# Optimization experiments

Measured on AMD Instinct MI355X. Metric: run time of the kernel, lower is better.

## Reference

```python
import jax, jax.numpy as jnp
import numpy as np

NEG = 0.01  # LeakyReLU negative_slope
N_NODES = 100000
N_EDGES = 400000
D = 128
IN_CH = 16
EDGE_DIM = 1


def _linear(x, w, b):
    # torch.nn.Linear convention: y = x @ W^T + b, W: [out, in]
    return x @ w.T + b


def setup_inputs() -> dict:
    key = jax.random.key(0)
    ks = jax.random.split(key, 32)

    def W(k, o, i):
        return jax.random.normal(k, (o, i), dtype=jnp.float32) * 0.02

    def B(k, o):
        return jax.random.normal(k, (o,), dtype=jnp.float32) * 0.02

    return {
        "x": jax.random.normal(ks[0], (N_NODES, IN_CH), dtype=jnp.float32),
        "edge_index": jax.random.randint(ks[1], (2, N_EDGES), 0, N_NODES, dtype=jnp.int64),
        "edge_weight": jax.random.uniform(ks[2], (N_EDGES, EDGE_DIM), dtype=jnp.float32),
        # prep MLP: in_ch -> 128 (LeakyReLU) -> 128 (Tanh)
        "prep_w0": W(ks[3], D, IN_CH), "prep_b0": B(ks[4], D),
        "prep_w1": W(ks[5], D, D), "prep_b1": B(ks[6], D),
        # GINEConv edge lin: edge_dim -> 128
        "edge_w": W(ks[7], D, EDGE_DIM), "edge_b": B(ks[8], D),
        # GINEConv nn: 128 -> 128 (LReLU) -> 128 (LReLU) -> 128 (Tanh)
        "mlp_w0": W(ks[9], D, D), "mlp_b0": B(ks[10], D),
        "mlp_w1": W(ks[11], D, D), "mlp_b1": B(ks[12], D),
        "mlp_w2": W(ks[13], D, D), "mlp_b2": B(ks[14], D),
        # post MLP: (128+128) -> 128 (LReLU) -> 64 (Tanh)
        "post_w0": W(ks[15], D, 2 * D), "post_b0": B(ks[16], D),
        "post_w1": W(ks[17], 64, D), "post_b1": B(ks[18], 64),
    }


def reference(x, edge_index, edge_weight,
              prep_w0, prep_b0, prep_w1, prep_b1,
              edge_w, edge_b,
              mlp_w0, mlp_b0, mlp_w1, mlp_b1, mlp_w2, mlp_b2,
              post_w0, post_b0, post_w1, post_b1):
    lrelu = lambda v: jax.nn.leaky_relu(v, negative_slope=NEG)
    n = x.shape[0]

    # sequential_prep
    h = lrelu(_linear(x, prep_w0, prep_b0))
    h = jnp.tanh(_linear(h, prep_w1, prep_b1))  # [N, D]

    r = h  # skip connection (x.clone())

    # GINEConv: message = relu(x_j + lin(edge_attr)); aggr = sum per dst
    e = _linear(edge_weight, edge_w, edge_b)            # [E, D]
    m = jax.nn.relu(h[edge_index[0]] + e)               # gather + edge add
    agg = jax.ops.segment_sum(m, edge_index[1], num_segments=n)  # scatter-sum
    z = h + agg  # (1 + eps) * x_i + aggr, eps = 0
    z = lrelu(_linear(z, mlp_w0, mlp_b0))
    z = lrelu(_linear(z, mlp_w1, mlp_b1))
    z = jnp.tanh(_linear(z, mlp_w2, mlp_b2))            # [N, D]

    # skip-cat
    h2 = jnp.concatenate([z, r], axis=1)                # [N, 2D]

    # sequential_post
    o = lrelu(_linear(h2, post_w0, post_b0))
    o = jnp.tanh(_linear(o, post_w1, post_b1))          # [N, 64]
    return o
```

## Files before the change

### kernel.cpp

```cpp
#include <hip/hip_runtime.h>

typedef short bf16x8 __attribute__((ext_vector_type(8)));
typedef float f32x4 __attribute__((ext_vector_type(4)));

#define NEG 0.01f

#define OFF_P0  0
#define OFF_P1  8192
#define OFF_M0  40960
#define OFF_Q0A 139264
#define OFF_Q0B 172032
#define OFF_Q1  204800
#define WBF_BYTES 221184

#define VMCNT0 asm volatile("s_waitcnt vmcnt(0)" ::: "memory")

__device__ __forceinline__ unsigned short f2bf(float f) {
  union { float f; unsigned u; } v; v.f = f;
  unsigned u = v.u;
  return (unsigned short)((u + 0x7fffu + ((u >> 16) & 1u)) >> 16);
}
__device__ __forceinline__ unsigned pack2(float a, float b) {
  return ((unsigned)f2bf(b) << 16) | (unsigned)f2bf(a);
}
__device__ __forceinline__ float bflo(unsigned u) { return __uint_as_float(u << 16); }
__device__ __forceinline__ float bfhi(unsigned u) { return __uint_as_float(u & 0xffff0000u); }
__device__ __forceinline__ float lrelu(float v) { return fmaxf(v, 0.0f) + NEG * fminf(v, 0.0f); }
__device__ __forceinline__ float tanh_fast(float x) {
  float e = __expf(2.0f * x);
  return 1.0f - __fdividef(2.0f, e + 1.0f);
}

__device__ __forceinline__ void gll16(const void* g, void* l) {
  __builtin_amdgcn_global_load_lds((const __attribute__((address_space(1))) void*)g,
                                   (__attribute__((address_space(3))) void*)l, 16, 0, 0);
}

__device__ __forceinline__ void gll_lin(const char* g, char* l, int nchunks, int wv, int nw, int lane) {
  for (int j = wv; j < nchunks; j += nw)
    gll16(g + j * 1024 + lane * 16, l + j * 1024 + lane * 16);
}

__device__ __forceinline__ void gll_rows(const char* gsrc, char* scr, int strip, int N, int lane) {
  #pragma unroll
  for (int c = 0; c < 8; ++c) {
    int L = c * 1024 + lane * 16;
    int row = strip + (L >> 8);
    row = row < N ? row : N - 1;
    gll16(gsrc + (size_t)row * 256 + (L & 255), scr + c * 1024 + lane * 16);
  }
}

__device__ __forceinline__ void copy_rows_out(const char* scr, char* gdst, int strip, int N, int lane) {
  #pragma unroll
  for (int c = 0; c < 8; ++c) {
    int L = c * 1024 + lane * 16;
    int row = strip + (L >> 8);
    if (row < N) *(uint4*)(gdst + (size_t)strip * 256 + L) = *(const uint4*)(scr + L);
  }
}

__device__ __forceinline__ void zacc82(f32x4 acc[8][2]) {
  #pragma unroll
  for (int m = 0; m < 8; ++m)
    #pragma unroll
    for (int n = 0; n < 2; ++n) { f32x4 z = {0.f,0.f,0.f,0.f}; acc[m][n] = z; }
}

__device__ __forceinline__ void gemm128(const char* wbase, const bf16x8 b[2][4],
                                        f32x4 acc[8][2], int l15, int lg) {
  __builtin_amdgcn_s_setprio(1);
  #pragma unroll
  for (int ks = 0; ks < 4; ++ks)
    #pragma unroll
    for (int mf = 0; mf < 8; ++mf) {
      const int row = 16*mf + l15;
      bf16x8 a = *(const bf16x8*)(wbase + row*256 + ((16*lg + 64*ks) ^ ((row&7)<<4)));
      acc[mf][0] = __builtin_amdgcn_mfma_f32_16x16x32_bf16(a, b[0][ks], acc[mf][0], 0,0,0);
      acc[mf][1] = __builtin_amdgcn_mfma_f32_16x16x32_bf16(a, b[1][ks], acc[mf][1], 0,0,0);
    }
  __builtin_amdgcn_s_setprio(0);
}

__device__ __forceinline__ void read_bfrags(const char* scr, bf16x8 b[2][4], int l15, int lg) {
  #pragma unroll
  for (int nf = 0; nf < 2; ++nf) {
    const int n = 16*nf + l15;
    #pragma unroll
    for (int ks = 0; ks < 4; ++ks)
      b[nf][ks] = *(const bf16x8*)(scr + n*256 + ((16*lg + 64*ks) ^ ((n&7)<<4)));
  }
}

template<int ACT>
__device__ __forceinline__ void ep_lds(const f32x4 acc[8][2], const float* __restrict__ bias,
                                       char* scr, int l15, int lg) {
  #pragma unroll
  for (int mf = 0; mf < 8; ++mf) {
    const int ch4 = 16*mf + 4*lg;
    const float4 bv = *(const float4*)(bias + ch4);
    #pragma unroll
    for (int nf = 0; nf < 2; ++nf) {
      const int n = 16*nf + l15;
      float v0 = acc[mf][nf][0]+bv.x, v1 = acc[mf][nf][1]+bv.y;
      float v2 = acc[mf][nf][2]+bv.z, v3 = acc[mf][nf][3]+bv.w;
      if (ACT == 0) { v0=lrelu(v0); v1=lrelu(v1); v2=lrelu(v2); v3=lrelu(v3); }
      else { v0=tanh_fast(v0); v1=tanh_fast(v1); v2=tanh_fast(v2); v3=tanh_fast(v3); }
      uint2 o = { pack2(v0,v1), pack2(v2,v3) };
      *(uint2*)(scr + n*256 + ((32*mf + 8*lg) ^ ((n&7)<<4))) = o;
    }
  }
}

extern "C" __global__ void __launch_bounds__(256) wpack_kernel(
    const float* __restrict__ pw0, const float* __restrict__ pw1,
    const float* __restrict__ mw0, const float* __restrict__ mw1, const float* __restrict__ mw2,
    const float* __restrict__ qw0, const float* __restrict__ qw1,
    char* wbf, int* deg, int N) {
  int gid = blockIdx.x * 256 + threadIdx.x;
  if (gid < 13824) {
    int c = gid;
    const float* src = nullptr;
    int dstB = 0;
    bool zero = false;
    if (c < 512) { int r = c >> 2, q = c & 3;
      dstB = OFF_P0 + r*64 + ((q*16) ^ ((r&3)<<4));
      if (q < 2) src = pw0 + r*16 + q*8; else zero = true;
    } else if (c < 2560) { int i = c - 512, r = i >> 4, q = i & 15;
      dstB = OFF_P1 + r*256 + ((q*16) ^ ((r&7)<<4));
      src = pw1 + r*128 + q*8;
    } else if (c < 8704) { int i = c - 2560, sl = i >> 11, j = i & 2047, r = j >> 4, q = j & 15;
      const float* m = (sl==0) ? mw0 : ((sl==1) ? mw1 : mw2);
      dstB = OFF_M0 + sl*32768 + r*256 + ((q*16) ^ ((r&7)<<4));
      src = m + r*128 + q*8;
    } else if (c < 10752) { int i = c - 8704, r = i >> 4, q = i & 15;
      dstB = OFF_Q0A + r*256 + ((q*16) ^ ((r&7)<<4));
      src = qw0 + r*256 + q*8;
    } else if (c < 12800) { int i = c - 10752, r = i >> 4, q = i & 15;
      dstB = OFF_Q0B + r*256 + ((q*16) ^ ((r&7)<<4));
      src = qw0 + r*256 + 128 + q*8;
    } else { int i = c - 12800, r = i >> 4, q = i & 15;
      dstB = OFF_Q1 + r*256 + ((q*16) ^ ((r&7)<<4));
      src = qw1 + r*128 + q*8;
    }
    ushort4 lo, hi;
    if (zero) { lo.x=lo.y=lo.z=lo.w=0; hi.x=hi.y=hi.z=hi.w=0; }
    else {
      float4 a = *(const float4*)src, b = *(const float4*)(src + 4);
      lo.x=f2bf(a.x); lo.y=f2bf(a.y); lo.z=f2bf(a.z); lo.w=f2bf(a.w);
      hi.x=f2bf(b.x); hi.y=f2bf(b.y); hi.z=f2bf(b.z); hi.w=f2bf(b.w);
    }
    *(ushort4*)(wbf + dstB) = lo;
    *(ushort4*)(wbf + dstB + 8) = hi;
  }
  if (gid < N) deg[gid] = 0;
}

extern "C" __global__ void __launch_bounds__(512) prep_kernel(
    const float* __restrict__ x,
    const float* __restrict__ pb0, const float* __restrict__ pb1,
    const char* __restrict__ wbf,
    const int* __restrict__ ei, int* deg, int E,
    char* hB, int N, int ntiles) {
  __shared__ char wP[40960];
  __shared__ char scr_all[8 * 8192];
  const int tid = threadIdx.x, lane = tid & 63, wv = tid >> 6;
  const int l15 = lane & 15, lg = lane >> 4;

  gll_lin(wbf + OFF_P0, wP, 40, wv, 8, lane);
  for (int e = blockIdx.x*512 + tid; e < E; e += gridDim.x*512)
    atomicAdd(&deg[ei[E + e]], 1);
  VMCNT0; __syncthreads();
  char* scr = scr_all + wv * 8192;

  for (int tile = blockIdx.x; tile < ntiles; tile += gridDim.x) {
    const int strip = tile*256 + wv*32;
    if (strip >= N) continue;
    bf16x8 bx[2];
    #pragma unroll
    for (int nf = 0; nf < 2; ++nf) {
      int node = strip + 16*nf + l15; node = node < N ? node : N-1;
      if (lg < 2) {
        float4 u = *(const float4*)(x + (size_t)node*16 + lg*8);
        float4 v = *(const float4*)(x + (size_t)node*16 + lg*8 + 4);
        bf16x8 t;
        t[0]=(short)f2bf(u.x); t[1]=(short)f2bf(u.y); t[2]=(short)f2bf(u.z); t[3]=(short)f2bf(u.w);
        t[4]=(short)f2bf(v.x); t[5]=(short)f2bf(v.y); t[6]=(short)f2bf(v.z); t[7]=(short)f2bf(v.w);
        bx[nf] = t;
      } else {
        bf16x8 t = {0,0,0,0,0,0,0,0}; bx[nf] = t;
      }
    }
    f32x4 acc[8][2];
    zacc82(acc);
    __builtin_amdgcn_s_setprio(1);
    #pragma unroll
    for (int mf = 0; mf < 8; ++mf) {
      const int row = 16*mf + l15;
      bf16x8 a = *(const bf16x8*)(wP + row*64 + ((16*lg) ^ ((row&3)<<4)));
      acc[mf][0] = __builtin_amdgcn_mfma_f32_16x16x32_bf16(a, bx[0], acc[mf][0], 0,0,0);
      acc[mf][1] = __builtin_amdgcn_mfma_f32_16x16x32_bf16(a, bx[1], acc[mf][1], 0,0,0);
    }
    __builtin_amdgcn_s_setprio(0);
    ep_lds<0>(acc, pb0, scr, l15, lg);
    bf16x8 b1[2][4];
    read_bfrags(scr, b1, l15, lg);
    zacc82(acc);
    gemm128(wP + 8192, b1, acc, l15, lg);
    ep_lds<1>(acc, pb1, scr, l15, lg);
    copy_rows_out(scr, hB, strip, N, lane);
  }
}

extern "C" __global__ void __launch_bounds__(256) scan_partials_kernel(
    const int* __restrict__ deg, int* partials, int N) {
  __shared__ int red[256];
  int b = blockIdx.x, t = threadIdx.x;
  int base = b * 2048 + t * 8, s = 0;
  #pragma unroll
  for (int i = 0; i < 8; ++i) { int idx = base + i; s += (idx < N) ? deg[idx] : 0; }
  red[t] = s; __syncthreads();
  for (int off = 128; off > 0; off >>= 1) {
    if (t < off) red[t] += red[t + off];
    __syncthreads();
  }
  if (t == 0) partials[b] = red[0];
}

extern "C" __global__ void scan_base_kernel(const int* __restrict__ partials, int* basearr, int nb) {
  int lane = threadIdx.x;
  int orig = (lane < nb) ? partials[lane] : 0;
  int v = orig;
  #pragma unroll
  for (int off = 1; off < 64; off <<= 1) {
    int u = __shfl_up(v, off);
    if (lane >= off) v += u;
  }
  if (lane < nb) basearr[lane] = v - orig;
}

extern "C" __global__ void __launch_bounds__(256) scan_apply_kernel(
    const int* __restrict__ deg, const int* __restrict__ basearr,
    int* offs, int* cur, int N) {
  __shared__ int sc[256];
  int b = blockIdx.x, t = threadIdx.x;
  int base = b * 2048 + t * 8;
  int loc[8], s = 0;
  #pragma unroll
  for (int i = 0; i < 8; ++i) { int idx = base + i; loc[i] = (idx < N) ? deg[idx] : 0; s += loc[i]; }
  sc[t] = s; __syncthreads();
  for (int off = 1; off < 256; off <<= 1) {
    int v = sc[t];
    int u = (t >= off) ? sc[t - off] : 0;
    __syncthreads();
    sc[t] = v + u;
    __syncthreads();
  }
  int run = basearr[b] + ((t == 0) ? 0 : sc[t - 1]);
  #pragma unroll
  for (int i = 0; i < 8; ++i) {
    int idx = base + i;
    if (idx < N) { offs[idx] = run; cur[idx] = run; run += loc[i]; }
  }
}

extern "C" __global__ void __launch_bounds__(256) scatter_kernel(
    const int* __restrict__ ei, const float* __restrict__ ew,
    int* cur, int2* recs, int E) {
  int e = blockIdx.x * 256 + threadIdx.x;
  if (e < E) {
    int dst = ei[E + e];
    int slot = atomicAdd(&cur[dst], 1);
    int2 r; r.x = ei[e]; r.y = __float_as_int(ew[e]);
    recs[slot] = r;
  }
}

extern "C" __global__ void __launch_bounds__(256) agg_kernel(
    const int* __restrict__ offs, const int* __restrict__ cur,
    const int2* __restrict__ recs,
    const float* __restrict__ elw, const float* __restrict__ elb,
    const char* __restrict__ hB, char* zB, int N) {
  const int lane = threadIdx.x & 63, wv = threadIdx.x >> 6;
  const int node = blockIdx.x * 4 + wv;
  if (node >= N) return;
  const float2 wl = *(const float2*)(elw + 2*lane);
  const float2 bl = *(const float2*)(elb + 2*lane);
  const int byteL = lane * 4;
  const int s = offs[node], e = cur[node];
  float c0 = 0.f, c1 = 0.f;
  int j = s;
  for (; j + 4 <= e; j += 4) {
    int2 r0 = recs[j], r1 = recs[j+1], r2 = recs[j+2], r3 = recs[j+3];
    unsigned u0 = *(const unsigned*)(hB + (size_t)r0.x*256 + (byteL ^ ((r0.x&7)<<4)));
    unsigned u1 = *(const unsigned*)(hB + (size_t)r1.x*256 + (byteL ^ ((r1.x&7)<<4)));
    unsigned u2 = *(const unsigned*)(hB + (size_t)r2.x*256 + (byteL ^ ((r2.x&7)<<4)));
    unsigned u3 = *(const unsigned*)(hB + (size_t)r3.x*256 + (byteL ^ ((r3.x&7)<<4)));
    float w0 = __int_as_float(r0.y), w1 = __int_as_float(r1.y);
    float w2 = __int_as_float(r2.y), w3 = __int_as_float(r3.y);
    c0 += fmaxf(bflo(u0) + w0*wl.x + bl.x, 0.f); c1 += fmaxf(bfhi(u0) + w0*wl.y + bl.y, 0.f);
    c0 += fmaxf(bflo(u1) + w1*wl.x + bl.x, 0.f); c1 += fmaxf(bfhi(u1) + w1*wl.y + bl.y, 0.f);
    c0 += fmaxf(bflo(u2) + w2*wl.x + bl.x, 0.f); c1 += fmaxf(bfhi(u2) + w2*wl.y + bl.y, 0.f);
    c0 += fmaxf(bflo(u3) + w3*wl.x + bl.x, 0.f); c1 += fmaxf(bfhi(u3) + w3*wl.y + bl.y, 0.f);
  }
  for (; j < e; ++j) {
    int2 r = recs[j];
    unsigned u = *(const unsigned*)(hB + (size_t)r.x*256 + (byteL ^ ((r.x&7)<<4)));
    float w = __int_as_float(r.y);
    c0 += fmaxf(bflo(u) + w*wl.x + bl.x, 0.f);
    c1 += fmaxf(bfhi(u) + w*wl.y + bl.y, 0.f);
  }
  unsigned hs = *(const unsigned*)(hB + (size_t)node*256 + (byteL ^ ((node&7)<<4)));
  unsigned o = pack2(bflo(hs) + c0, bfhi(hs) + c1);
  *(unsigned*)(zB + (size_t)node*256 + (byteL ^ ((node&7)<<4))) = o;
}

extern "C" __global__ void __launch_bounds__(448) nodeA_kernel(
    const char* __restrict__ zB, const char* __restrict__ wbf,
    const float* __restrict__ mb0, const float* __restrict__ mb1, const float* __restrict__ mb2,
    char* z3, int N, int ntiles) {
  __shared__ char wM[98304];
  __shared__ char scr_all[7 * 8192];
  const int tid = threadIdx.x, lane = tid & 63, wv = tid >> 6;
  const int l15 = lane & 15, lg = lane >> 4;

  gll_lin(wbf + OFF_M0, wM, 96, wv, 7, lane);
  VMCNT0; __syncthreads();
  char* scr = scr_all + wv * 8192;

  for (int tile = blockIdx.x; tile < ntiles; tile += gridDim.x) {
    const int strip = tile*224 + wv*32;
    if (strip >= N) continue;
    gll_rows(zB, scr, strip, N, lane);
    VMCNT0;
    bf16x8 b0[2][4];
    read_bfrags(scr, b0, l15, lg);
    f32x4 acc[8][2];
    zacc82(acc);
    gemm128(wM, b0, acc, l15, lg);
    ep_lds<0>(acc, mb0, scr, l15, lg);
    bf16x8 b1[2][4];
    read_bfrags(scr, b1, l15, lg);
    zacc82(acc);
    gemm128(wM + 32768, b1, acc, l15, lg);
    ep_lds<0>(acc, mb1, scr, l15, lg);
    bf16x8 b2[2][4];
    read_bfrags(scr, b2, l15, lg);
    zacc82(acc);
    gemm128(wM + 65536, b2, acc, l15, lg);
    ep_lds<1>(acc, mb2, scr, l15, lg);
    copy_rows_out(scr, z3, strip, N, lane);
  }
}

extern "C" __global__ void __launch_bounds__(512) nodeB_kernel(
    const char* __restrict__ z3, const char* hB, const char* __restrict__ wbf,
    const float* __restrict__ qb0, const float* __restrict__ qb1,
    float* out, int N, int ntiles) {
  __shared__ char wQ[81920];
  __shared__ char scr_all[8 * 8192];
  const int tid = threadIdx.x, lane = tid & 63, wv = tid >> 6;
  const int l15 = lane & 15, lg = lane >> 4;

  gll_lin(wbf + OFF_Q0A, wQ, 80, wv, 8, lane);
  VMCNT0; __syncthreads();
  char* scr = scr_all + wv * 8192;

  for (int tile = blockIdx.x; tile < ntiles; tile += gridDim.x) {
    const int strip = tile*256 + wv*32;
    if (strip >= N) continue;
    gll_rows(z3, scr, strip, N, lane);
    bf16x8 bh[2][4];
    #pragma unroll
    for (int nf = 0; nf < 2; ++nf) {
      int node = strip + 16*nf + l15; node = node < N ? node : N-1;
      const char* hr = hB + (size_t)node*256;
      const int sw = (node&7) << 4;
      #pragma unroll
      for (int ks = 0; ks < 4; ++ks)
        bh[nf][ks] = *(const bf16x8*)(hr + ((16*lg + 64*ks) ^ sw));
    }
    VMCNT0;
    bf16x8 bz[2][4];
    read_bfrags(scr, bz, l15, lg);
    f32x4 acc[8][2];
    zacc82(acc);
    gemm128(wQ, bz, acc, l15, lg);
    gemm128(wQ + 32768, bh, acc, l15, lg);
    ep_lds<0>(acc, qb0, scr, l15, lg);

    bf16x8 bt[2][4];
    read_bfrags(scr, bt, l15, lg);
    f32x4 a2[4][2];
    #pragma unroll
    for (int m = 0; m < 4; ++m)
      #pragma unroll
      for (int n = 0; n < 2; ++n) { f32x4 z = {0.f,0.f,0.f,0.f}; a2[m][n] = z; }
    __builtin_amdgcn_s_setprio(1);
    #pragma unroll
    for (int ks = 0; ks < 4; ++ks)
      #pragma unroll
      for (int mf = 0; mf < 4; ++mf) {
        const int row = 16*mf + l15;
        bf16x8 a = *(const bf16x8*)(wQ + 65536 + row*256 + ((16*lg + 64*ks) ^ ((row&7)<<4)));
        a2[mf][0] = __builtin_amdgcn_mfma_f32_16x16x32_bf16(a, bt[0][ks], a2[mf][0], 0,0,0);
        a2[mf][1] = __builtin_amdgcn_mfma_f32_16x16x32_bf16(a, bt[1][ks], a2[mf][1], 0,0,0);
      }
    __builtin_amdgcn_s_setprio(0);
    #pragma unroll
    for (int mf = 0; mf < 4; ++mf) {
      const int ch4 = 16*mf + 4*lg;
      const float4 bv = *(const float4*)(qb1 + ch4);
      #pragma unroll
      for (int nf = 0; nf < 2; ++nf) {
        const int node = strip + 16*nf + l15;
        if (node < N) {
          float4 o;
          o.x = tanh_fast(a2[mf][nf][0] + bv.x);
          o.y = tanh_fast(a2[mf][nf][1] + bv.y);
          o.z = tanh_fast(a2[mf][nf][2] + bv.z);
          o.w = tanh_fast(a2[mf][nf][3] + bv.w);
          *(float4*)(out + (size_t)node*64 + ch4) = o;
        }
      }
    }
  }
}

extern "C" void kernel_launch(void* const* d_in, const int* in_sizes, int n_in,
                              void* d_out, int out_size, void* d_ws, size_t ws_size,
                              hipStream_t stream) {
  const float* x   = (const float*)d_in[0];
  const int*   ei  = (const int*)d_in[1];
  const float* ew  = (const float*)d_in[2];
  const float* pw0 = (const float*)d_in[3];
  const float* pb0 = (const float*)d_in[4];
  const float* pw1 = (const float*)d_in[5];
  const float* pb1 = (const float*)d_in[6];
  const float* elw = (const float*)d_in[7];
  const float* elb = (const float*)d_in[8];
  const float* mw0 = (const float*)d_in[9];
  const float* mb0 = (const float*)d_in[10];
  const float* mw1 = (const float*)d_in[11];
  const float* mb1 = (const float*)d_in[12];
  const float* mw2 = (const float*)d_in[13];
  const float* mb2 = (const float*)d_in[14];
  const float* qw0 = (const float*)d_in[15];
  const float* qb0 = (const float*)d_in[16];
  const float* qw1 = (const float*)d_in[17];
  const float* qb1 = (const float*)d_in[18];
  float* out = (float*)d_out;

  const int N = in_sizes[0] / 16;
  const int E = in_sizes[1] / 2;

  char* p = (char*)d_ws;
  auto alloc = [&](size_t bytes) { char* r = p; p += (bytes + 255) & ~(size_t)255; return r; };
  const size_t rowBytes = (size_t)N * 256;

  char* zB      = alloc(rowBytes);
  char* z3      = alloc(rowBytes);
  int2* recs    = (int2*)alloc((size_t)E * 8);
  int*  deg     = (int*)alloc((size_t)N * 4);
  int*  offs    = (int*)alloc((size_t)N * 4);
  int*  cur     = (int*)alloc((size_t)N * 4);
  int*  part    = (int*)alloc(256 * 4);
  int*  basearr = (int*)alloc(256 * 4);
  char* wbf     = alloc(WBF_BYTES);

  char* hB;
  if ((size_t)(p - (char*)d_ws) + rowBytes <= ws_size) {
    hB = alloc(rowBytes);
  } else {
    hB = (char*)d_out;
  }

  const int ntilesP = (N + 255) / 256;
  const int ntilesA = (N + 223) / 224;
  const int ntilesB = (N + 255) / 256;
  const int nb1  = (N + 2047) / 2048;
  const int eblk = (E + 255) / 256;
  const int pgrid = ((13824 > N ? 13824 : N) + 255) / 256;

  wpack_kernel<<<dim3(pgrid), dim3(256), 0, stream>>>(pw0, pw1, mw0, mw1, mw2, qw0, qw1,
                                                      wbf, deg, N);
  prep_kernel<<<dim3(256), dim3(512), 0, stream>>>(x, pb0, pb1, wbf, ei, deg, E, hB, N, ntilesP);
  scan_partials_kernel<<<dim3(nb1), dim3(256), 0, stream>>>(deg, part, N);
  scan_base_kernel<<<dim3(1), dim3(64), 0, stream>>>(part, basearr, nb1);
  scan_apply_kernel<<<dim3(nb1), dim3(256), 0, stream>>>(deg, basearr, offs, cur, N);
  scatter_kernel<<<dim3(eblk), dim3(256), 0, stream>>>(ei, ew, cur, recs, E);
  agg_kernel<<<dim3((N + 3) / 4), dim3(256), 0, stream>>>(offs, cur, recs, elw, elb, hB, zB, N);
  nodeA_kernel<<<dim3(256), dim3(448), 0, stream>>>(zB, wbf, mb0, mb1, mb2, z3, N, ntilesA);
  nodeB_kernel<<<dim3(256), dim3(512), 0, stream>>>(z3, hB, wbf, qb0, qb1, out, N, ntilesB);
}
```

Measured before the change: 259.3 us.

## Remove scan_base kernel, reshape prep grid, and aggregate two nodes per wave

```diff
diff --git a/kernel.cpp b/kernel.cpp
--- a/kernel.cpp
+++ b/kernel.cpp
@@ -156,60 +156,59 @@
   if (gid < N) deg[gid] = 0;
 }
 
-extern "C" __global__ void __launch_bounds__(512) prep_kernel(
+extern "C" __global__ void __launch_bounds__(256, 2) prep_kernel(
     const float* __restrict__ x,
     const float* __restrict__ pb0, const float* __restrict__ pb1,
     const char* __restrict__ wbf,
     const int* __restrict__ ei, int* deg, int E,
-    char* hB, int N, int ntiles) {
+    char* hB, int N) {
   __shared__ char wP[40960];
-  __shared__ char scr_all[8 * 8192];
+  __shared__ char scr_all[4 * 8192];
   const int tid = threadIdx.x, lane = tid & 63, wv = tid >> 6;
   const int l15 = lane & 15, lg = lane >> 4;
 
-  gll_lin(wbf + OFF_P0, wP, 40, wv, 8, lane);
-  for (int e = blockIdx.x*512 + tid; e < E; e += gridDim.x*512)
+  gll_lin(wbf + OFF_P0, wP, 40, wv, 4, lane);
+  for (int e = blockIdx.x*256 + tid; e < E; e += gridDim.x*256)
     atomicAdd(&deg[ei[E + e]], 1);
   VMCNT0; __syncthreads();
   char* scr = scr_all + wv * 8192;
 
-  for (int tile = blockIdx.x; tile < ntiles; tile += gridDim.x) {
-    const int strip = tile*256 + wv*32;
-    if (strip >= N) continue;
-    bf16x8 bx[2];
-    #pragma unroll
-    for (int nf = 0; nf < 2; ++nf) {
-      int node = strip + 16*nf + l15; node = node < N ? node : N-1;
-      if (lg < 2) {
-        float4 u = *(const float4*)(x + (size_t)node*16 + lg*8);
-        float4 v = *(const float4*)(x + (size_t)node*16 + lg*8 + 4);
-        bf16x8 t;
-        t[0]=(short)f2bf(u.x); t[1]=(short)f2bf(u.y); t[2]=(short)f2bf(u.z); t[3]=(short)f2bf(u.w);
-        t[4]=(short)f2bf(v.x); t[5]=(short)f2bf(v.y); t[6]=(short)f2bf(v.z); t[7]=(short)f2bf(v.w);
-        bx[nf] = t;
-      } else {
-        bf16x8 t = {0,0,0,0,0,0,0,0}; bx[nf] = t;
-      }
-    }
-    f32x4 acc[8][2];
-    zacc82(acc);
-    __builtin_amdgcn_s_setprio(1);
-    #pragma unroll
-    for (int mf = 0; mf < 8; ++mf) {
-      const int row = 16*mf + l15;
-      bf16x8 a = *(const bf16x8*)(wP + row*64 + ((16*lg) ^ ((row&3)<<4)));
-      acc[mf][0] = __builtin_amdgcn_mfma_f32_16x16x32_bf16(a, bx[0], acc[mf][0], 0,0,0);
-      acc[mf][1] = __builtin_amdgcn_mfma_f32_16x16x32_bf16(a, bx[1], acc[mf][1], 0,0,0);
-    }
-    __builtin_amdgcn_s_setprio(0);
-    ep_lds<0>(acc, pb0, scr, l15, lg);
-    bf16x8 b1[2][4];
-    read_bfrags(scr, b1, l15, lg);
-    zacc82(acc);
-    gemm128(wP + 8192, b1, acc, l15, lg);
-    ep_lds<1>(acc, pb1, scr, l15, lg);
-    copy_rows_out(scr, hB, strip, N, lane);
-  }
+  const int strip = blockIdx.x*128 + wv*32;
+  if (strip >= N) return;
+
+  bf16x8 bx[2];
+  #pragma unroll
+  for (int nf = 0; nf < 2; ++nf) {
+    int node = strip + 16*nf + l15; node = node < N ? node : N-1;
+    if (lg < 2) {
+      float4 u = *(const float4*)(x + (size_t)node*16 + lg*8);
+      float4 v = *(const float4*)(x + (size_t)node*16 + lg*8 + 4);
+      bf16x8 t;
+      t[0]=(short)f2bf(u.x); t[1]=(short)f2bf(u.y); t[2]=(short)f2bf(u.z); t[3]=(short)f2bf(u.w);
+      t[4]=(short)f2bf(v.x); t[5]=(short)f2bf(v.y); t[6]=(short)f2bf(v.z); t[7]=(short)f2bf(v.w);
+      bx[nf] = t;
+    } else {
+      bf16x8 t = {0,0,0,0,0,0,0,0}; bx[nf] = t;
+    }
+  }
+  f32x4 acc[8][2];
+  zacc82(acc);
+  __builtin_amdgcn_s_setprio(1);
+  #pragma unroll
+  for (int mf = 0; mf < 8; ++mf) {
+    const int row = 16*mf + l15;
+    bf16x8 a = *(const bf16x8*)(wP + row*64 + ((16*lg) ^ ((row&3)<<4)));
+    acc[mf][0] = __builtin_amdgcn_mfma_f32_16x16x32_bf16(a, bx[0], acc[mf][0], 0,0,0);
+    acc[mf][1] = __builtin_amdgcn_mfma_f32_16x16x32_bf16(a, bx[1], acc[mf][1], 0,0,0);
+  }
+  __builtin_amdgcn_s_setprio(0);
+  ep_lds<0>(acc, pb0, scr, l15, lg);
+  bf16x8 b1[2][4];
+  read_bfrags(scr, b1, l15, lg);
+  zacc82(acc);
+  gemm128(wP + 8192, b1, acc, l15, lg);
+  ep_lds<1>(acc, pb1, scr, l15, lg);
+  copy_rows_out(scr, hB, strip, N, lane);
 }
 
 extern "C" __global__ void __launch_bounds__(256) scan_partials_kernel(
@@ -227,23 +226,18 @@
   if (t == 0) partials[b] = red[0];
 }
 
-extern "C" __global__ void scan_base_kernel(const int* __restrict__ partials, int* basearr, int nb) {
-  int lane = threadIdx.x;
-  int orig = (lane < nb) ? partials[lane] : 0;
-  int v = orig;
-  #pragma unroll
-  for (int off = 1; off < 64; off <<= 1) {
-    int u = __shfl_up(v, off);
-    if (lane >= off) v += u;
-  }
-  if (lane < nb) basearr[lane] = v - orig;
-}
-
 extern "C" __global__ void __launch_bounds__(256) scan_apply_kernel(
-    const int* __restrict__ deg, const int* __restrict__ basearr,
-    int* offs, int* cur, int N) {
+    const int* __restrict__ deg, const int* __restrict__ partials,
+    int* offs, int* cur, int N, int nb) {
   __shared__ int sc[256];
+  __shared__ int baseSh;
   int b = blockIdx.x, t = threadIdx.x;
+  if (t < 64) {
+    int v = (t < b && t < nb) ? partials[t] : 0;
+    #pragma unroll
+    for (int off = 32; off > 0; off >>= 1) v += __shfl_xor(v, off);
+    if (t == 0) baseSh = v;
+  }
   int base = b * 2048 + t * 8;
   int loc[8], s = 0;
   #pragma unroll
@@ -256,7 +250,7 @@
     sc[t] = v + u;
     __syncthreads();
   }
-  int run = basearr[b] + ((t == 0) ? 0 : sc[t - 1]);
+  int run = baseSh + ((t == 0) ? 0 : sc[t - 1]);
   #pragma unroll
   for (int i = 0; i < 8; ++i) {
     int idx = base + i;
@@ -282,37 +276,44 @@
     const float* __restrict__ elw, const float* __restrict__ elb,
     const char* __restrict__ hB, char* zB, int N) {
   const int lane = threadIdx.x & 63, wv = threadIdx.x >> 6;
-  const int node = blockIdx.x * 4 + wv;
+  const int half = lane >> 5, l31 = lane & 31;
+  const int node = blockIdx.x * 8 + wv * 2 + half;
   if (node >= N) return;
-  const float2 wl = *(const float2*)(elw + 2*lane);
-  const float2 bl = *(const float2*)(elb + 2*lane);
-  const int byteL = lane * 4;
+  const float4 wl = *(const float4*)(elw + 4*l31);
+  const float4 bl = *(const float4*)(elb + 4*l31);
+  const int byteL = l31 * 8;
   const int s = offs[node], e = cur[node];
-  float c0 = 0.f, c1 = 0.f;
+  float c0 = 0.f, c1 = 0.f, c2 = 0.f, c3 = 0.f;
   int j = s;
-  for (; j + 4 <= e; j += 4) {
-    int2 r0 = recs[j], r1 = recs[j+1], r2 = recs[j+2], r3 = recs[j+3];
-    unsigned u0 = *(const unsigned*)(hB + (size_t)r0.x*256 + (byteL ^ ((r0.x&7)<<4)));
-    unsigned u1 = *(const unsigned*)(hB + (size_t)r1.x*256 + (byteL ^ ((r1.x&7)<<4)));
-    unsigned u2 = *(const unsigned*)(hB + (size_t)r2.x*256 + (byteL ^ ((r2.x&7)<<4)));
-    unsigned u3 = *(const unsigned*)(hB + (size_t)r3.x*256 + (byteL ^ ((r3.x&7)<<4)));
+  for (; j + 2 <= e; j += 2) {
+    int2 r0 = recs[j], r1 = recs[j+1];
+    uint2 u0 = *(const uint2*)(hB + (size_t)r0.x*256 + (byteL ^ ((r0.x&7)<<4)));
+    uint2 u1 = *(const uint2*)(hB + (size_t)r1.x*256 + (byteL ^ ((r1.x&7)<<4)));
     float w0 = __int_as_float(r0.y), w1 = __int_as_float(r1.y);
-    float w2 = __int_as_float(r2.y), w3 = __int_as_float(r3.y);
-    c0 += fmaxf(bflo(u0) + w0*wl.x + bl.x, 0.f); c1 += fmaxf(bfhi(u0) + w0*wl.y + bl.y, 0.f);
-    c0 += fmaxf(bflo(u1) + w1*wl.x + bl.x, 0.f); c1 += fmaxf(bfhi(u1) + w1*wl.y + bl.y, 0.f);
-    c0 += fmaxf(bflo(u2) + w2*wl.x + bl.x, 0.f); c1 += fmaxf(bfhi(u2) + w2*wl.y + bl.y, 0.f);
-    c0 += fmaxf(bflo(u3) + w3*wl.x + bl.x, 0.f); c1 += fmaxf(bfhi(u3) + w3*wl.y + bl.y, 0.f);
-  }
-  for (; j < e; ++j) {
+    c0 += fmaxf(bflo(u0.x) + w0*wl.x + bl.x, 0.f);
+    c1 += fmaxf(bfhi(u0.x) + w0*wl.y + bl.y, 0.f);
+    c2 += fmaxf(bflo(u0.y) + w0*wl.z + bl.z, 0.f);
+    c3 += fmaxf(bfhi(u0.y) + w0*wl.w + bl.w, 0.f);
+    c0 += fmaxf(bflo(u1.x) + w1*wl.x + bl.x, 0.f);
+    c1 += fmaxf(bfhi(u1.x) + w1*wl.y + bl.y, 0.f);
+    c2 += fmaxf(bflo(u1.y) + w1*wl.z + bl.z, 0.f);
+    c3 += fmaxf(bfhi(u1.y) + w1*wl.w + bl.w, 0.f);
+  }
+  if (j < e) {
     int2 r = recs[j];
-    unsigned u = *(const unsigned*)(hB + (size_t)r.x*256 + (byteL ^ ((r.x&7)<<4)));
+    uint2 u = *(const uint2*)(hB + (size_t)r.x*256 + (byteL ^ ((r.x&7)<<4)));
     float w = __int_as_float(r.y);
-    c0 += fmaxf(bflo(u) + w*wl.x + bl.x, 0.f);
-    c1 += fmaxf(bfhi(u) + w*wl.y + bl.y, 0.f);
-  }
-  unsigned hs = *(const unsigned*)(hB + (size_t)node*256 + (byteL ^ ((node&7)<<4)));
-  unsigned o = pack2(bflo(hs) + c0, bfhi(hs) + c1);
-  *(unsigned*)(zB + (size_t)node*256 + (byteL ^ ((node&7)<<4))) = o;
+    c0 += fmaxf(bflo(u.x) + w*wl.x + bl.x, 0.f);
+    c1 += fmaxf(bfhi(u.x) + w*wl.y + bl.y, 0.f);
+    c2 += fmaxf(bflo(u.y) + w*wl.z + bl.z, 0.f);
+    c3 += fmaxf(bfhi(u.y) + w*wl.w + bl.w, 0.f);
+  }
+  const int swz = byteL ^ ((node&7)<<4);
+  uint2 hs = *(const uint2*)(hB + (size_t)node*256 + swz);
+  uint2 o;
+  o.x = pack2(bflo(hs.x) + c0, bfhi(hs.x) + c1);
+  o.y = pack2(bflo(hs.y) + c2, bfhi(hs.y) + c3);
+  *(uint2*)(zB + (size_t)node*256 + swz) = o;
 }
 
 extern "C" __global__ void __launch_bounds__(448) nodeA_kernel(
@@ -465,7 +466,6 @@
   int*  offs    = (int*)alloc((size_t)N * 4);
   int*  cur     = (int*)alloc((size_t)N * 4);
   int*  part    = (int*)alloc(256 * 4);
-  int*  basearr = (int*)alloc(256 * 4);
   char* wbf     = alloc(WBF_BYTES);
 
   char* hB;
@@ -475,7 +475,7 @@
     hB = (char*)d_out;
   }
 
-  const int ntilesP = (N + 255) / 256;
+  const int pblk    = (N + 127) / 128;
   const int ntilesA = (N + 223) / 224;
   const int ntilesB = (N + 255) / 256;
   const int nb1  = (N + 2047) / 2048;
@@ -484,12 +484,11 @@
 
   wpack_kernel<<<dim3(pgrid), dim3(256), 0, stream>>>(pw0, pw1, mw0, mw1, mw2, qw0, qw1,
                                                       wbf, deg, N);
-  prep_kernel<<<dim3(256), dim3(512), 0, stream>>>(x, pb0, pb1, wbf, ei, deg, E, hB, N, ntilesP);
+  prep_kernel<<<dim3(pblk), dim3(256), 0, stream>>>(x, pb0, pb1, wbf, ei, deg, E, hB, N);
   scan_partials_kernel<<<dim3(nb1), dim3(256), 0, stream>>>(deg, part, N);
-  scan_base_kernel<<<dim3(1), dim3(64), 0, stream>>>(part, basearr, nb1);
-  scan_apply_kernel<<<dim3(nb1), dim3(256), 0, stream>>>(deg, basearr, offs, cur, N);
+  scan_apply_kernel<<<dim3(nb1), dim3(256), 0, stream>>>(deg, part, offs, cur, N, nb1);
   scatter_kernel<<<dim3(eblk), dim3(256), 0, stream>>>(ei, ew, cur, recs, E);
-  agg_kernel<<<dim3((N + 3) / 4), dim3(256), 0, stream>>>(offs, cur, recs, elw, elb, hB, zB, N);
+  agg_kernel<<<dim3((N + 7) / 8), dim3(256), 0, stream>>>(offs, cur, recs, elw, elb, hB, zB, N);
   nodeA_kernel<<<dim3(256), dim3(448), 0, stream>>>(zB, wbf, mb0, mb1, mb2, z3, N, ntilesA);
   nodeB_kernel<<<dim3(256), dim3(512), 0, stream>>>(z3, hB, wbf, qb0, qb1, out, N, ntilesB);
 }
```

Measured after the change: 244.1 us. 5.9% less time.
